# Performance work log

Measured on AMD Instinct MI355X. Metric: run time of the kernel, lower is better.

The kernel has to match this reference:

```python
import jax, jax.numpy as jnp
import numpy as np

# Segmented tensor product, uniform-1d case (subscripts 'u,u,u'):
#   out[z, idx_out[p]*u:(idx_out[p]+1)*u] += coeffs[p] * x0_seg[z, idx0[p]] * x1_seg[z, idx1[p]]
U = 128          # mode extent 'u'
NSEG = (32, 8, 32)  # segments per operand (in0, in1, out)
P = 128          # number of paths
Z = 16384        # batch


def setup_inputs() -> dict:
    key = jax.random.key(0)
    k0, k1, k2, k3, k4, k5 = jax.random.split(key, 6)
    return {
        "x0": jax.random.normal(k0, (Z, NSEG[0] * U), dtype=jnp.float32),
        "x1": jax.random.normal(k1, (Z, NSEG[1] * U), dtype=jnp.float32),
        "coeffs": jax.random.normal(k2, (P,), dtype=jnp.float32),
        "idx0": jax.random.randint(k3, (P,), 0, NSEG[0], dtype=jnp.int32),
        "idx1": jax.random.randint(k4, (P,), 0, NSEG[1], dtype=jnp.int32),
        "idx_out": jax.random.randint(k5, (P,), 0, NSEG[2], dtype=jnp.int32),
    }


def reference(x0, x1, coeffs, idx0, idx1, idx_out):
    z = x0.shape[0]
    x0r = x0.reshape(z, NSEG[0], U)  # [Z, n0, u]
    x1r = x1.reshape(z, NSEG[1], U)  # [Z, n1, u]
    # gather the segment used by each path: [Z, P, u]
    s0 = x0r[:, idx0, :]
    s1 = x1r[:, idx1, :]
    # per-path contribution, elementwise over u (coefficient subscript is scalar)
    contrib = (s0 * s1) * coeffs[None, :, None]          # [Z, P, u]
    # scatter-add paths into output segments
    contrib = jnp.transpose(contrib, (1, 0, 2))          # [P, Z, u]
    out_seg = jax.ops.segment_sum(contrib, idx_out, num_segments=NSEG[2])  # [n2, Z, u]
    return jnp.transpose(out_seg, (1, 0, 2)).reshape(z, NSEG[2] * U)
```

## Files before the change

### kernel.cpp

```cpp
#include <hip/hip_runtime.h>


#define Z_DIM 16384
#define U_DIM 128
#define NSEG0 32
#define NSEG1 8
#define NSEG2 32
#define P_DIM 128
#define BLK   512

#define X0_FLOATS (NSEG0 * U_DIM)
#define X1_FLOATS (NSEG1 * U_DIM)

#define META_BASE 40
#define BLOB_INTS 304

typedef float f32x4 __attribute__((ext_vector_type(4)));

__global__ __launch_bounds__(128) void tp_setup(
    const float* __restrict__ coeffs,
    const int* __restrict__ idx0,
    const int* __restrict__ idx1,
    const int* __restrict__ idx_out,
    int* __restrict__ blob)
{
    __shared__ int s_cnt[NSEG2];
    __shared__ int s_off[NSEG2 + 1];
    const int t = threadIdx.x;
    if (t < NSEG2) s_cnt[t] = 0;
    __syncthreads();
    const int o = idx_out[t];
    const int r = atomicAdd(&s_cnt[o], 1);
    __syncthreads();
    if (t == 0) {
        int sum = 0;
        for (int i = 0; i < NSEG2; ++i) { s_off[i] = sum; sum += s_cnt[i]; }
        s_off[NSEG2] = sum;
    }
    __syncthreads();
    const int d = s_off[o] + r;
    int2* meta = reinterpret_cast<int2*>(blob + META_BASE);
    meta[d] = make_int2((idx0[t] * (U_DIM * 4)) | ((idx1[t] * (U_DIM * 4)) << 16),
                        __float_as_int(coeffs[t]));
    if (t <= NSEG2) blob[t] = s_off[t];
    if (t >= 33 && t < META_BASE) blob[t] = 0;
    if (t >= 296 && t < BLOB_INTS) blob[t] = 0;
}

__global__ __launch_bounds__(BLK, 8) void tp_kernel(
    const float* __restrict__ x0,
    const float* __restrict__ x1,
    const int* __restrict__ blob_g,
    float* __restrict__ out)
{
    __shared__ float s_x0[X0_FLOATS];
    __shared__ float s_x1[X1_FLOATS];
    __shared__ int   s_blob[BLOB_INTS];

    const int t = threadIdx.x;
    const size_t z = (size_t)blockIdx.x;

    {
        const float4* g0 = reinterpret_cast<const float4*>(x0 + z * (size_t)X0_FLOATS);
        const float4* g1 = reinterpret_cast<const float4*>(x1 + z * (size_t)X1_FLOATS);
        const float4* gb = reinterpret_cast<const float4*>(blob_g);
        float4* l0 = reinterpret_cast<float4*>(s_x0);
        float4* l1 = reinterpret_cast<float4*>(s_x1);
        float4* lb = reinterpret_cast<float4*>(s_blob);
        #pragma unroll
        for (int i = 0; i < (X0_FLOATS / 4) / BLK; ++i)
            __builtin_amdgcn_global_load_lds(
                (const __attribute__((address_space(1))) void*)(g0 + i * BLK + t),
                (__attribute__((address_space(3))) void*)(l0 + i * BLK + t),
                16, 0, 0);
        if (t < X1_FLOATS / 4)
            __builtin_amdgcn_global_load_lds(
                (const __attribute__((address_space(1))) void*)(g1 + t),
                (__attribute__((address_space(3))) void*)(l1 + t),
                16, 0, 0);
        if (t < BLOB_INTS / 4)
            __builtin_amdgcn_global_load_lds(
                (const __attribute__((address_space(1))) void*)(gb + t),
                (__attribute__((address_space(3))) void*)(lb + t),
                16, 0, 0);
    }
    __syncthreads();

    const int w  = t >> 6;
    const int h  = (t >> 5) & 1;
    const int uq = t & 31;

    const int seg0 = 4 * w + 2 * h;
    const char* x0base = reinterpret_cast<const char*>(s_x0 + uq * 4);
    const char* x1base = reinterpret_cast<const char*>(s_x1 + uq * 4);
    const int2* s_meta = reinterpret_cast<const int2*>(s_blob + META_BASE);
    float* orow = out + z * (NSEG2 * U_DIM) + uq * 4;

    const int b = s_blob[seg0];
    const int m = s_blob[seg0 + 1];
    const int e = s_blob[seg0 + 2];

    int sb = b;
    #pragma unroll
    for (int oo = 0; oo < 2; ++oo) {
        const int se = (oo == 0) ? m : e;
        f32x4 acc = (f32x4)0.f;
        int2 mt = s_meta[sb];
        for (int k = sb; k < se; ++k) {
            const int2 mn = s_meta[k + 1];
            const float c = __int_as_float(mt.y);
            const f32x4 a = *reinterpret_cast<const f32x4*>(x0base + (mt.x & 0xffff));
            const f32x4 v = *reinterpret_cast<const f32x4*>(x1base + ((unsigned)mt.x >> 16));
            acc += a * v * c;
            mt = mn;
        }
        __builtin_nontemporal_store(acc,
            reinterpret_cast<f32x4*>(orow + (seg0 + oo) * U_DIM));
        sb = se;
    }
}

extern "C" void kernel_launch(void* const* d_in, const int* in_sizes, int n_in,
                              void* d_out, int out_size, void* d_ws, size_t ws_size,
                              hipStream_t stream) {
    const float* x0      = (const float*)d_in[0];
    const float* x1      = (const float*)d_in[1];
    const float* coeffs  = (const float*)d_in[2];
    const int*   idx0    = (const int*)d_in[3];
    const int*   idx1    = (const int*)d_in[4];
    const int*   idx_out = (const int*)d_in[5];
    float* out = (float*)d_out;

    int* blob = (int*)d_ws;

    tp_setup<<<1, P_DIM, 0, stream>>>(coeffs, idx0, idx1, idx_out, blob);
    tp_kernel<<<Z_DIM, BLK, 0, stream>>>(x0, x1, blob, out);
}
```

Measured before the change: 109.4 us.

## Convert tensor-product kernel to persistent blocks with double-buffered LDS prefetch

Replaces the one-block-per-batch-row launch with a fixed grid of persistent blocks that loop over rows with a grid stride. Each block stages the next row's x0/x1 into a second LDS buffer through async global-to-LDS loads while computing the current row. This is meant to overlap load latency with compute and remove per-block launch and setup overhead. In exchange it doubles LDS per block and runs only a few blocks per CU, which lowers occupancy on a kernel that is already close to memory-bandwidth bound.

```diff
diff --git a/kernel.cpp b/kernel.cpp
--- a/kernel.cpp
+++ b/kernel.cpp
@@ -8,9 +8,11 @@
 #define NSEG2 32
 #define P_DIM 128
 #define BLK   512
+#define NBLOCKS 768
 
 #define X0_FLOATS (NSEG0 * U_DIM)
 #define X1_FLOATS (NSEG1 * U_DIM)
+#define BUF_FLOATS (X0_FLOATS + X1_FLOATS)
 
 #define META_BASE 40
 #define BLOB_INTS 304
@@ -47,76 +49,89 @@
     if (t >= 296 && t < BLOB_INTS) blob[t] = 0;
 }
 
+__device__ __forceinline__ void stage_tile(const float* __restrict__ x0,
+                                           const float* __restrict__ x1,
+                                           float* lbuf, size_t z, int t)
+{
+    const float4* g0 = reinterpret_cast<const float4*>(x0 + z * (size_t)X0_FLOATS);
+    const float4* g1 = reinterpret_cast<const float4*>(x1 + z * (size_t)X1_FLOATS);
+    float4* l0 = reinterpret_cast<float4*>(lbuf);
+    float4* l1 = reinterpret_cast<float4*>(lbuf + X0_FLOATS);
+    #pragma unroll
+    for (int i = 0; i < (X0_FLOATS / 4) / BLK; ++i)
+        __builtin_amdgcn_global_load_lds(
+            (const __attribute__((address_space(1))) void*)(g0 + i * BLK + t),
+            (__attribute__((address_space(3))) void*)(l0 + i * BLK + t),
+            16, 0, 0);
+    if (t < X1_FLOATS / 4)
+        __builtin_amdgcn_global_load_lds(
+            (const __attribute__((address_space(1))) void*)(g1 + t),
+            (__attribute__((address_space(3))) void*)(l1 + t),
+            16, 0, 0);
+}
+
 __global__ __launch_bounds__(BLK, 8) void tp_kernel(
     const float* __restrict__ x0,
     const float* __restrict__ x1,
     const int* __restrict__ blob_g,
     float* __restrict__ out)
 {
-    __shared__ float s_x0[X0_FLOATS];
-    __shared__ float s_x1[X1_FLOATS];
+    __shared__ float buf[2][BUF_FLOATS];
     __shared__ int   s_blob[BLOB_INTS];
 
     const int t = threadIdx.x;
-    const size_t z = (size_t)blockIdx.x;
 
     {
-        const float4* g0 = reinterpret_cast<const float4*>(x0 + z * (size_t)X0_FLOATS);
-        const float4* g1 = reinterpret_cast<const float4*>(x1 + z * (size_t)X1_FLOATS);
         const float4* gb = reinterpret_cast<const float4*>(blob_g);
-        float4* l0 = reinterpret_cast<float4*>(s_x0);
-        float4* l1 = reinterpret_cast<float4*>(s_x1);
         float4* lb = reinterpret_cast<float4*>(s_blob);
-        #pragma unroll
-        for (int i = 0; i < (X0_FLOATS / 4) / BLK; ++i)
-            __builtin_amdgcn_global_load_lds(
-                (const __attribute__((address_space(1))) void*)(g0 + i * BLK + t),
-                (__attribute__((address_space(3))) void*)(l0 + i * BLK + t),
-                16, 0, 0);
-        if (t < X1_FLOATS / 4)
-            __builtin_amdgcn_global_load_lds(
-                (const __attribute__((address_space(1))) void*)(g1 + t),
-                (__attribute__((address_space(3))) void*)(l1 + t),
-                16, 0, 0);
         if (t < BLOB_INTS / 4)
             __builtin_amdgcn_global_load_lds(
                 (const __attribute__((address_space(1))) void*)(gb + t),
                 (__attribute__((address_space(3))) void*)(lb + t),
                 16, 0, 0);
     }
-    __syncthreads();
+    stage_tile(x0, x1, &buf[0][0], (size_t)blockIdx.x, t);
 
     const int w  = t >> 6;
     const int h  = (t >> 5) & 1;
     const int uq = t & 31;
+    const int seg0 = 4 * w + 2 * h;
 
-    const int seg0 = 4 * w + 2 * h;
-    const char* x0base = reinterpret_cast<const char*>(s_x0 + uq * 4);
-    const char* x1base = reinterpret_cast<const char*>(s_x1 + uq * 4);
-    const int2* s_meta = reinterpret_cast<const int2*>(s_blob + META_BASE);
-    float* orow = out + z * (NSEG2 * U_DIM) + uq * 4;
+    int cur = 0;
+    for (int tile = blockIdx.x; tile < Z_DIM; tile += NBLOCKS) {
+        __syncthreads();
 
-    const int b = s_blob[seg0];
-    const int m = s_blob[seg0 + 1];
-    const int e = s_blob[seg0 + 2];
+        if (tile + NBLOCKS < Z_DIM)
+            stage_tile(x0, x1, &buf[cur ^ 1][0], (size_t)(tile + NBLOCKS), t);
 
-    int sb = b;
-    #pragma unroll
-    for (int oo = 0; oo < 2; ++oo) {
-        const int se = (oo == 0) ? m : e;
-        f32x4 acc = (f32x4)0.f;
-        int2 mt = s_meta[sb];
-        for (int k = sb; k < se; ++k) {
-            const int2 mn = s_meta[k + 1];
-            const float c = __int_as_float(mt.y);
-            const f32x4 a = *reinterpret_cast<const f32x4*>(x0base + (mt.x & 0xffff));
-            const f32x4 v = *reinterpret_cast<const f32x4*>(x1base + ((unsigned)mt.x >> 16));
-            acc += a * v * c;
-            mt = mn;
+        const char* x0base = reinterpret_cast<const char*>(&buf[cur][uq * 4]);
+        const char* x1base = reinterpret_cast<const char*>(&buf[cur][X0_FLOATS + uq * 4]);
+        const int2* s_meta = reinterpret_cast<const int2*>(s_blob + META_BASE);
+        float* orow = out + (size_t)tile * (NSEG2 * U_DIM) + uq * 4;
+
+        const int b = s_blob[seg0];
+        const int m = s_blob[seg0 + 1];
+        const int e = s_blob[seg0 + 2];
+
+        int sb = b;
+        #pragma unroll
+        for (int oo = 0; oo < 2; ++oo) {
+            const int se = (oo == 0) ? m : e;
+            f32x4 acc = (f32x4)0.f;
+            int2 mt = s_meta[sb];
+            for (int k = sb; k < se; ++k) {
+                const int2 mn = s_meta[k + 1];
+                const float c = __int_as_float(mt.y);
+                const f32x4 a = *reinterpret_cast<const f32x4*>(x0base + (mt.x & 0xffff));
+                const f32x4 v = *reinterpret_cast<const f32x4*>(x1base + ((unsigned)mt.x >> 16));
+                acc += a * v * c;
+                mt = mn;
+            }
+            __builtin_nontemporal_store(acc,
+                reinterpret_cast<f32x4*>(orow + (seg0 + oo) * U_DIM));
+            sb = se;
         }
-        __builtin_nontemporal_store(acc,
-            reinterpret_cast<f32x4*>(orow + (seg0 + oo) * U_DIM));
-        sb = se;
+        cur ^= 1;
     }
 }
 
@@ -134,5 +149,5 @@
     int* blob = (int*)d_ws;
 
     tp_setup<<<1, P_DIM, 0, stream>>>(coeffs, idx0, idx1, idx_out, blob);
-    tp_kernel<<<Z_DIM, BLK, 0, stream>>>(x0, x1, blob, out);
+    tp_kernel<<<NBLOCKS, BLK, 0, stream>>>(x0, x1, blob, out);
 }
```

After: 115.7 us. 5.8% more time.
